# Kernel tuning notes

Hardware: AMD Instinct MI355X
Metric: run time of the kernel (lower is better)

The kernel has to match this reference:

```python
import jax, jax.numpy as jnp
import numpy as np

N = 100000   # nodes
E = 3200000  # edges (avg degree 32)
IN = 512
HID = 128
OUT = 128


def setup_inputs() -> dict:
    key = jax.random.key(0)
    ks = jax.random.split(key, 9)
    x = jax.random.normal(ks[0], (N, IN), dtype=jnp.float32)
    edge_index = jax.random.randint(ks[1], (2, E), 0, N, dtype=jnp.int32)
    perm = jax.random.permutation(ks[2], N).astype(jnp.int32)
    # GCN layer params (glorot-ish scaling)
    W1 = jax.random.normal(ks[3], (IN, HID), jnp.float32) / np.sqrt(IN)
    b1 = jnp.zeros((HID,), jnp.float32)
    W2 = jax.random.normal(ks[4], (HID, OUT), jnp.float32) / np.sqrt(HID)
    b2 = jnp.zeros((OUT,), jnp.float32)
    # nn.Bilinear(OUT, OUT, 1): weight [1, OUT, OUT], bias [1]
    Wd = jax.random.normal(ks[5], (1, OUT, OUT), jnp.float32) / np.sqrt(OUT)
    bd = jnp.zeros((1,), jnp.float32)
    return {"x": x, "edge_index": edge_index, "perm": perm,
            "W1": W1, "b1": b1, "W2": W2, "b2": b2, "Wd": Wd, "bd": bd}


def gcn_conv(x, W, b, src, dst, n):
    """PyG GCNConv: add self-loops, symmetric deg^-1/2 norm, linear, scatter-add, bias."""
    h = x @ W  # [N, out]
    loops = jnp.arange(n, dtype=src.dtype)
    s = jnp.concatenate([src, loops])
    d = jnp.concatenate([dst, loops])
    deg = jax.ops.segment_sum(jnp.ones(d.shape, x.dtype), d, num_segments=n)
    dinv = jnp.where(deg > 0, jax.lax.rsqrt(deg), 0.0)
    norm = dinv[s] * dinv[d]                      # [E+N]
    msg = h[s] * norm[:, None]                     # gather + scale
    out = jax.ops.segment_sum(msg, d, num_segments=n)  # scatter-add to dst
    return out + b


def encode(x, W1, b1, W2, b2, src, dst, n):
    h = jax.nn.relu(gcn_conv(x, W1, b1, src, dst, n))
    return gcn_conv(h, W2, b2, src, dst, n)


def reference(x, edge_index, perm, W1, b1, W2, b2, Wd, bd):
    n = x.shape[0]
    src, dst = edge_index[0], edge_index[1]
    H = encode(x, W1, b1, W2, b2, src, dst, n)          # [N, OUT]
    s = jax.nn.sigmoid(jnp.mean(H, axis=0))             # [OUT]
    # Bilinear disc against broadcasted summary: pos[n] = H[n] @ Wd[0] @ s + bd
    Ws = Wd[0] @ s                                      # [OUT]
    pos = (H @ Ws)[:, None] + bd                        # [N, 1]
    Hc = encode(x[perm], W1, b1, W2, b2, src, dst, n)
    neg = (Hc @ Ws)[:, None] + bd                       # [N, 1]
    return pos, neg
```

## Files before the change

kernel.cpp:

```cpp
#include <hip/hip_runtime.h>
#include <hip/hip_bf16.h>

typedef unsigned int uint;
typedef unsigned short ushort;
typedef __attribute__((ext_vector_type(8))) short bf16x8;
typedef __attribute__((ext_vector_type(4))) float f32x4;

static __device__ __forceinline__ ushort f2bf(float f) {
    uint u = __builtin_bit_cast(uint, f);
    return (ushort)((u + 0x7FFFu + ((u >> 16) & 1u)) >> 16);
}
static __device__ __forceinline__ uint pk2(float lo, float hi) {
    return (uint)f2bf(lo) | ((uint)f2bf(hi) << 16);
}
static __device__ __forceinline__ float bflo(uint u) { return __builtin_bit_cast(float, u << 16); }
static __device__ __forceinline__ float bfhi(uint u) { return __builtin_bit_cast(float, u & 0xFFFF0000u); }


#define CS_G 512

__global__ __launch_bounds__(256) void part_hist_dual(
        const int* __restrict__ src, const int* __restrict__ dst,
        uint* __restrict__ counts, int E, int NB, int chunk) {
    __shared__ uint h0[512], h1[512];
    int t = threadIdx.x;
    for (int b = t; b < 512; b += 256) { h0[b] = 0; h1[b] = 0; }
    __syncthreads();
    int s0 = blockIdx.x * chunk;
    int s1 = min(s0 + chunk, E);
    int i = s0 + t * 4;
    for (; i + 4 <= s1; i += 1024) {
        int4 d4 = *(const int4*)(dst + i);
        int4 s4 = *(const int4*)(src + i);
        atomicAdd(&h0[d4.x >> 8], 1u); atomicAdd(&h0[d4.y >> 8], 1u);
        atomicAdd(&h0[d4.z >> 8], 1u); atomicAdd(&h0[d4.w >> 8], 1u);
        atomicAdd(&h1[s4.x >> 8], 1u); atomicAdd(&h1[s4.y >> 8], 1u);
        atomicAdd(&h1[s4.z >> 8], 1u); atomicAdd(&h1[s4.w >> 8], 1u);
    }
    for (int k = i; k < min(i + 4, s1); ++k) {
        atomicAdd(&h0[dst[k] >> 8], 1u);
        atomicAdd(&h1[src[k] >> 8], 1u);
    }
    __syncthreads();
    for (int b = t; b < NB; b += 256) {
        counts[(size_t)b * CS_G + blockIdx.x] = h0[b];
        counts[(size_t)(NB + b) * CS_G + blockIdx.x] = h1[b];
    }
}

__global__ __launch_bounds__(256) void part_scatter_dual(
        const int* __restrict__ src, const int* __restrict__ dst,
        const uint* __restrict__ scn, uint* __restrict__ rec,
        int E, int NB, int chunk) {
    __shared__ uint cur0[512], cur1[512];
    int t = threadIdx.x;
    for (int b = t; b < NB; b += 256) {
        cur0[b] = scn[(size_t)b * CS_G + blockIdx.x];
        cur1[b] = scn[(size_t)(NB + b) * CS_G + blockIdx.x];
    }
    __syncthreads();
    int s0 = blockIdx.x * chunk;
    int s1 = min(s0 + chunk, E);
    int i = s0 + t * 4;
    for (; i + 4 <= s1; i += 1024) {
        int4 d4 = *(const int4*)(dst + i);
        int4 s4 = *(const int4*)(src + i);
        int dd[4] = {d4.x, d4.y, d4.z, d4.w};
        int ss[4] = {s4.x, s4.y, s4.z, s4.w};
#pragma unroll
        for (int k = 0; k < 4; ++k) {
            uint slotD = atomicAdd(&cur0[dd[k] >> 8], 1u);
            rec[slotD] = ((uint)(dd[k] & 255) << 24) | (uint)ss[k];
            uint slotS = atomicAdd(&cur1[ss[k] >> 8], 1u);
            rec[slotS] = ((uint)(ss[k] & 255) << 24) | (uint)dd[k];
        }
    }
    for (int k = i; k < min(i + 4, s1); ++k) {
        int d = dst[k], s = src[k];
        uint slotD = atomicAdd(&cur0[d >> 8], 1u);
        rec[slotD] = ((uint)(d & 255) << 24) | (uint)s;
        uint slotS = atomicAdd(&cur1[s >> 8], 1u);
        rec[slotS] = ((uint)(s & 255) << 24) | (uint)d;
    }
}

__global__ __launch_bounds__(256) void bucket_build(
        const uint* __restrict__ scn, const uint* __restrict__ rec,
        int* __restrict__ rp, int* __restrict__ adj,
        float* __restrict__ dinv, int NB, int n) {
    __shared__ uint cnt[256];
    __shared__ uint sc[2][256];
    int b = blockIdx.x, t = threadIdx.x;
    uint base = scn[(size_t)b * CS_G];
    uint bend = scn[(size_t)(b + 1) * CS_G];
    cnt[t] = 0;
    __syncthreads();
    for (uint i = base + t; i < bend; i += 256)
        atomicAdd(&cnt[rec[i] >> 24], 1u);
    __syncthreads();
    uint vcnt = cnt[t];
    float dv = rsqrtf((float)(vcnt + 1));
    sc[0][t] = vcnt;
    __syncthreads();
    int pb = 0;
    for (int off = 1; off < 256; off <<= 1) {
        uint add = (t >= off) ? sc[pb][t - off] : 0u;
        sc[pb ^ 1][t] = sc[pb][t] + add;
        pb ^= 1;
        __syncthreads();
    }
    uint excl = sc[pb][t] - vcnt;
    uint off0 = base + excl;
    int vtx = b * 256 + t;
    if (vtx < n) {
        rp[vtx] = (int)off0;
        dinv[vtx] = dv;
    }
    if (b == 0 && t == 0) rp[n] = (int)scn[(size_t)NB * CS_G];
    cnt[t] = off0;
    __syncthreads();
    for (uint i = base + t; i < bend; i += 256) {
        uint r = rec[i];
        uint slot = atomicAdd(&cnt[r >> 24], 1u);
        adj[slot] = (int)(r & 0xFFFFFFu);
    }
}

__global__ __launch_bounds__(256) void bucket_tw(
        const uint* __restrict__ scn, const uint* __restrict__ rec,
        const float* __restrict__ dinv, float* __restrict__ tv,
        int NB, int n) {
    __shared__ float tw_sh[256];
    int b = blockIdx.x, t = threadIdx.x;
    uint base = scn[(size_t)(NB + b) * CS_G];
    uint bend = scn[(size_t)(NB + b + 1) * CS_G];
    tw_sh[t] = 0.f;
    __syncthreads();
    for (uint i = base + t; i < bend; i += 256) {
        uint r = rec[i];
        atomicAdd(&tw_sh[r >> 24], dinv[r & 0xFFFFFFu]);
    }
    __syncthreads();
    int vtx = b * 256 + t;
    if (vtx < n) {
        float dv = dinv[vtx];
        tv[vtx] = dv * (tw_sh[t] + dv);
    }
}


#define SC_T 256
#define SC_C 1024

__global__ void scan_part(const int* __restrict__ deg, int* __restrict__ bsum, int n) {
    __shared__ int sh[SC_T];
    int t = threadIdx.x;
    int base = blockIdx.x * SC_C;
    int s = 0;
    for (int i = 0; i < 4; i++) {
        int idx = base + t * 4 + i;
        if (idx < n) s += deg[idx];
    }
    sh[t] = s;
    __syncthreads();
    for (int off = 128; off > 0; off >>= 1) {
        if (t < off) sh[t] += sh[t + off];
        __syncthreads();
    }
    if (t == 0) bsum[blockIdx.x] = sh[0];
}

__global__ void scan_block(int* bsum, int nb, int* total) {
    __shared__ int sh[256];
    int t = threadIdx.x;
    int v[4];
    int s = 0;
#pragma unroll
    for (int i = 0; i < 4; i++) {
        int idx = t * 4 + i;
        v[i] = (idx < nb) ? bsum[idx] : 0;
        s += v[i];
    }
    sh[t] = s;
    __syncthreads();
    for (int off = 1; off < 256; off <<= 1) {
        int u = (t >= off) ? sh[t - off] : 0;
        __syncthreads();
        sh[t] += u;
        __syncthreads();
    }
    int excl = sh[t] - s;
#pragma unroll
    for (int i = 0; i < 4; i++) {
        int idx = t * 4 + i;
        if (idx < nb) { bsum[idx] = excl; excl += v[i]; }
    }
    if (t == 255) *total = sh[255];
}

__global__ void scan_write(const int* __restrict__ deg, const int* __restrict__ bsum,
                           const int* __restrict__ total, int* __restrict__ rp, int n) {
    __shared__ int sh[SC_T];
    int t = threadIdx.x;
    int base = blockIdx.x * SC_C;
    int vals[4];
    int s = 0;
    for (int i = 0; i < 4; i++) {
        int idx = base + t * 4 + i;
        vals[i] = (idx < n) ? deg[idx] : 0;
        s += vals[i];
    }
    sh[t] = s;
    __syncthreads();
    for (int off = 1; off < SC_T; off <<= 1) {
        int v = (t >= off) ? sh[t - off] : 0;
        __syncthreads();
        sh[t] += v;
        __syncthreads();
    }
    int excl = sh[t] - s + bsum[blockIdx.x];
    for (int i = 0; i < 4; i++) {
        int idx = base + t * 4 + i;
        if (idx < n) { rp[idx] = excl; excl += vals[i]; }
    }
    if (blockIdx.x == 0 && t == 0) rp[n] = *total;
}


__global__ void pack_w(const float* __restrict__ W, ushort* __restrict__ Wp) {
    int kc = blockIdx.x >> 3, n = blockIdx.x & 7;
    int l = threadIdx.x;
    ushort o[8];
#pragma unroll
    for (int j = 0; j < 8; ++j) {
        float v = W[(size_t)(kc * 32 + ((l >> 4) * 8) + j) * 128 + n * 16 + (l & 15)];
        o[j] = f2bf(v);
    }
    uint4 pk;
    pk.x = (uint)o[0] | ((uint)o[1] << 16);
    pk.y = (uint)o[2] | ((uint)o[3] << 16);
    pk.z = (uint)o[4] | ((uint)o[5] << 16);
    pk.w = (uint)o[6] | ((uint)o[7] << 16);
    *(uint4*)(Wp + ((size_t)(kc * 8 + n) * 64 + l) * 8) = pk;
}


__global__ __launch_bounds__(256) void gemm1_mfma(
        const float* __restrict__ X, const ushort* __restrict__ Wp,
        ushort* __restrict__ Cb, int M, int K) {
    __shared__ ushort As[2][64][40];
    int t = threadIdx.x, lane = t & 63, w = t >> 6;
    int brow = blockIdx.x * 64;
    int KC = K >> 5;
    f32x4 acc[8] = {};
    int sr = t >> 2, sk = (t & 3) * 8;
    int gr = brow + sr;
    bool xok = gr < M;
    int frow = w * 16 + (lane & 15);
    int fk = (lane >> 4) * 8;

    auto loadpk = [&](int kc) -> uint4 {
        float4 xa = make_float4(0.f, 0.f, 0.f, 0.f), xb = xa;
        if (xok) {
            const float* xp = X + (size_t)gr * K + kc * 32 + sk;
            xa = *(const float4*)xp;
            xb = *(const float4*)(xp + 4);
        }
        uint4 pk;
        pk.x = pk2(xa.x, xa.y);
        pk.y = pk2(xa.z, xa.w);
        pk.z = pk2(xb.x, xb.y);
        pk.w = pk2(xb.z, xb.w);
        return pk;
    };

    uint4 cur = loadpk(0);
    int buf = 0;
    for (int kc = 0; kc < KC; ++kc) {
        *(uint4*)&As[buf][sr][sk] = cur;
        __syncthreads();
        if (kc + 1 < KC) cur = loadpk(kc + 1);
        bf16x8 af = *(const bf16x8*)&As[buf][frow][fk];
        const ushort* wbase = Wp + ((size_t)(kc * 8) * 64 + lane) * 8;
#pragma unroll
        for (int n = 0; n < 8; ++n) {
            bf16x8 bfr = *(const bf16x8*)(wbase + (size_t)n * 64 * 8);
            acc[n] = __builtin_amdgcn_mfma_f32_16x16x32_bf16(af, bfr, acc[n], 0, 0, 0);
        }
        buf ^= 1;
    }
    int colbase = lane & 15;
    int rowbase = brow + w * 16 + ((lane >> 4) << 2);
#pragma unroll
    for (int n = 0; n < 8; ++n) {
#pragma unroll
        for (int r = 0; r < 4; ++r) {
            int grr = rowbase + r;
            if (grr < M) Cb[(size_t)grr * 128 + n * 16 + colbase] = f2bf(acc[n][r]);
        }
    }
}


#define ACC8(acc, g, w)                                   \
    acc[0] += bflo(g.x) * w; acc[1] += bfhi(g.x) * w;     \
    acc[2] += bflo(g.y) * w; acc[3] += bfhi(g.y) * w;     \
    acc[4] += bflo(g.z) * w; acc[5] += bfhi(g.z) * w;     \
    acc[6] += bflo(g.w) * w; acc[7] += bfhi(g.w) * w;

__global__ __launch_bounds__(256) void prop_b0(
        const ushort* __restrict__ A,
        const int* __restrict__ rp, const int* __restrict__ adj,
        const float* __restrict__ dinv, const float* __restrict__ tv,
        const float* __restrict__ bias,
        ushort* __restrict__ B, float* __restrict__ mparts, int n) {
    __shared__ float msum[128];
    int t = threadIdx.x;
    if (t < 128) msum[t] = 0.f;
    __syncthreads();
    int wave = (blockIdx.x * blockDim.x + t) >> 6;
    int lane = t & 63;
    int q = lane >> 4, l = lane & 15;
    int v = wave * 4 + q;
    bool vok = v < n;
    int vc = vok ? v : (n - 1);
    float dv = dinv[vc];

    uint4 r0 = *(const uint4*)(A + (size_t)vc * 128 + 8 * l);
    float a0[8];
    a0[0] = bflo(r0.x) * dv; a0[1] = bfhi(r0.x) * dv;
    a0[2] = bflo(r0.y) * dv; a0[3] = bfhi(r0.y) * dv;
    a0[4] = bflo(r0.z) * dv; a0[5] = bfhi(r0.z) * dv;
    a0[6] = bflo(r0.w) * dv; a0[7] = bfhi(r0.w) * dv;

    int i = rp[vc], end = rp[vc + 1];
    int un[4];
#pragma unroll
    for (int k = 0; k < 4; ++k) un[k] = (i + k < end) ? adj[i + k] : vc;

    while (__ballot(i < end)) {
        int uc[4];
#pragma unroll
        for (int k = 0; k < 4; ++k) uc[k] = un[k];
        uint4 g0[4];
#pragma unroll
        for (int k = 0; k < 4; ++k) g0[k] = *(const uint4*)(A + (size_t)uc[k] * 128 + 8 * l);
        float du[4];
#pragma unroll
        for (int k = 0; k < 4; ++k) du[k] = (i + k < end) ? dinv[uc[k]] : 0.f;
        i += 4;
#pragma unroll
        for (int k = 0; k < 4; ++k) un[k] = (i + k < end) ? adj[i + k] : vc;
#pragma unroll
        for (int k = 0; k < 4; ++k) {
            float w = du[k];
            ACC8(a0, g0[k], w)
        }
    }
    float4 bA = *(const float4*)(bias + 8 * l);
    float4 bB = *(const float4*)(bias + 8 * l + 4);
    float bb[8] = {bA.x, bA.y, bA.z, bA.w, bB.x, bB.y, bB.z, bB.w};
#pragma unroll
    for (int j = 0; j < 8; ++j)
        a0[j] = fmaxf(a0[j] * dv + bb[j], 0.f);
    if (vok) {
        uint4 o;
        o.x = pk2(a0[0], a0[1]); o.y = pk2(a0[2], a0[3]);
        o.z = pk2(a0[4], a0[5]); o.w = pk2(a0[6], a0[7]);
        *(uint4*)(B + (size_t)v * 128 + 8 * l) = o;
    }
    float tvv = vok ? tv[vc] : 0.f;
#pragma unroll
    for (int j = 0; j < 8; ++j)
        atomicAdd(&msum[8 * l + j], tvv * a0[j]);
    __syncthreads();
    if (t < 128)
        atomicAdd(&mparts[(size_t)(blockIdx.x & 31) * 128 + t], msum[t]);
}


__global__ __launch_bounds__(256) void prop_b1(
        const ushort* __restrict__ A, const ushort* __restrict__ B,
        const int* __restrict__ rp, const int* __restrict__ adj,
        const float* __restrict__ dinv, const int* __restrict__ perm,
        const float* __restrict__ bias, const float* __restrict__ w2s,
        float2* __restrict__ cpair, int n) {
    int wave = (blockIdx.x * blockDim.x + threadIdx.x) >> 6;
    int lane = threadIdx.x & 63;
    int q = lane >> 4, l = lane & 15;
    int v = wave * 4 + q;
    bool vok = v < n;
    int vc = vok ? v : (n - 1);
    float dv = dinv[vc];
    int self = perm[vc];

    uint4 r1 = *(const uint4*)(A + (size_t)self * 128 + 8 * l);
    float a1[8];
    a1[0] = bflo(r1.x) * dv; a1[1] = bfhi(r1.x) * dv;
    a1[2] = bflo(r1.y) * dv; a1[3] = bfhi(r1.y) * dv;
    a1[4] = bflo(r1.z) * dv; a1[5] = bfhi(r1.z) * dv;
    a1[6] = bflo(r1.w) * dv; a1[7] = bfhi(r1.w) * dv;

    int i = rp[vc], end = rp[vc + 1];
    int un[4];
#pragma unroll
    for (int k = 0; k < 4; ++k) un[k] = (i + k < end) ? adj[i + k] : vc;

    while (__ballot(i < end)) {
        int uc[4];
#pragma unroll
        for (int k = 0; k < 4; ++k) uc[k] = un[k];
        int uu[4];
#pragma unroll
        for (int k = 0; k < 4; ++k) uu[k] = perm[uc[k]];
        uint4 g1[4];
#pragma unroll
        for (int k = 0; k < 4; ++k) g1[k] = *(const uint4*)(A + (size_t)uu[k] * 128 + 8 * l);
        float du[4];
#pragma unroll
        for (int k = 0; k < 4; ++k) du[k] = (i + k < end) ? dinv[uc[k]] : 0.f;
        i += 4;
#pragma unroll
        for (int k = 0; k < 4; ++k) un[k] = (i + k < end) ? adj[i + k] : vc;
#pragma unroll
        for (int k = 0; k < 4; ++k) {
            float w = du[k];
            ACC8(a1, g1[k], w)
        }
    }
    if (!vok) return;
    float4 bA = *(const float4*)(bias + 8 * l);
    float4 bB = *(const float4*)(bias + 8 * l + 4);
    float bb[8] = {bA.x, bA.y, bA.z, bA.w, bB.x, bB.y, bB.z, bB.w};
    float4 wA = *(const float4*)(w2s + 8 * l);
    float4 wB = *(const float4*)(w2s + 8 * l + 4);
    float ww[8] = {wA.x, wA.y, wA.z, wA.w, wB.x, wB.y, wB.z, wB.w};
    float c1 = 0.f;
#pragma unroll
    for (int j = 0; j < 8; ++j)
        c1 += fmaxf(a1[j] * dv + bb[j], 0.f) * ww[j];
    uint4 b0 = *(const uint4*)(B + (size_t)vc * 128 + 8 * l);
    float c0 = bflo(b0.x) * ww[0] + bfhi(b0.x) * ww[1]
             + bflo(b0.y) * ww[2] + bfhi(b0.y) * ww[3]
             + bflo(b0.z) * ww[4] + bfhi(b0.z) * ww[5]
             + bflo(b0.w) * ww[6] + bfhi(b0.w) * ww[7];
#pragma unroll
    for (int off = 1; off < 16; off <<= 1) {
        c0 += __shfl_xor(c0, off);
        c1 += __shfl_xor(c1, off);
    }
    if (l == 0) cpair[v] = make_float2(dv * c0, dv * c1);
}


__global__ void tiny_chain(const float* __restrict__ mparts, const float* __restrict__ W2,
                           const float* __restrict__ b2, const float* __restrict__ Wd,
                           const float* __restrict__ bd,
                           float* __restrict__ w2s, float* __restrict__ k0, int n) {
    __shared__ float mB[128];
    __shared__ float s_sh[128];
    __shared__ float ws_sh[128];
    __shared__ float red[128];
    int t = threadIdx.x;
    float acc = 0.f;
    for (int r = 0; r < 32; ++r) acc += mparts[(size_t)r * 128 + t];
    mB[t] = acc;
    __syncthreads();
    acc = 0.f;
    for (int k = 0; k < 128; ++k) acc += mB[k] * W2[k * 128 + t];
    float m = acc / (float)n + b2[t];
    s_sh[t] = 1.f / (1.f + expf(-m));
    __syncthreads();
    acc = 0.f;
    for (int j = 0; j < 128; ++j) acc += Wd[t * 128 + j] * s_sh[j];
    ws_sh[t] = acc;
    __syncthreads();
    acc = 0.f;
    for (int j = 0; j < 128; ++j) acc += W2[t * 128 + j] * ws_sh[j];
    w2s[t] = acc;
    red[t] = b2[t] * ws_sh[t];
    __syncthreads();
    for (int off = 64; off > 0; off >>= 1) {
        if (t < off) red[t] += red[t + off];
        __syncthreads();
    }
    if (t == 0) *k0 = red[0] + bd[0];
}

__global__ __launch_bounds__(256) void sprop(
        const float2* __restrict__ cpair,
        const int* __restrict__ rp, const int* __restrict__ adj,
        const float* __restrict__ dinv, const float* __restrict__ k0,
        float* __restrict__ out, int n) {
    int wave = (blockIdx.x * blockDim.x + threadIdx.x) >> 6;
    int lane = threadIdx.x & 63;
    int q = lane >> 4, l = lane & 15;
    int v = wave * 4 + q;
    if (v >= n) return;
    float a0 = 0.f, a1 = 0.f;
    int beg = rp[v], end = rp[v + 1];
    for (int i = beg + l; i < end; i += 16) {
        float2 c = cpair[adj[i]];
        a0 += c.x;
        a1 += c.y;
    }
#pragma unroll
    for (int off = 1; off < 16; off <<= 1) {
        a0 += __shfl_xor(a0, off);
        a1 += __shfl_xor(a1, off);
    }
    if (l == 0) {
        float dv = dinv[v];
        float kk = *k0;
        float2 cs = cpair[v];
        out[v] = dv * (a0 + cs.x) + kk;
        out[n + v] = dv * (a1 + cs.y) + kk;
    }
}


extern "C" void kernel_launch(void* const* d_in, const int* in_sizes, int n_in,
                              void* d_out, int out_size, void* d_ws, size_t ws_size,
                              hipStream_t stream) {
    const float* x  = (const float*)d_in[0];
    const int*   ei = (const int*)d_in[1];
    const int* perm = (const int*)d_in[2];
    const float* W1 = (const float*)d_in[3];
    const float* b1 = (const float*)d_in[4];
    const float* W2 = (const float*)d_in[5];
    const float* b2 = (const float*)d_in[6];
    const float* Wd = (const float*)d_in[7];
    const float* bd = (const float*)d_in[8];

    const int N = in_sizes[2];
    const int E = in_sizes[1] / 2;
    const int IN = in_sizes[0] / N;
    const int* src = ei;
    const int* dst = ei + E;
    float* out = (float*)d_out;

    const int NB = (N + 255) >> 8;
    const int M2 = 2 * NB * CS_G;
    int chunk = (E + CS_G - 1) / CS_G;
    chunk = (chunk + 3) & ~3;

    char* p = (char*)d_ws;
    auto alloc = [&](size_t bytes) -> void* {
        void* r = (void*)p;
        p += (bytes + 511) & ~(size_t)511;
        return r;
    };
    float* mparts = (float*)alloc(32 * 128 * 4);
    uint*  counts = (uint*)alloc((size_t)M2 * 4);
    uint*  scn    = (uint*)alloc((size_t)(M2 + 1) * 4);
    uint*  rec    = (uint*)alloc((size_t)2 * E * 4);
    int*   rp     = (int*)alloc((size_t)(N + 1) * 4);
    int*   adj    = (int*)alloc((size_t)E * 4);
    float* dinv   = (float*)alloc((size_t)N * 4);
    float* tvv    = (float*)alloc((size_t)N * 4);
    int*   bsum   = (int*)alloc(4096);
    int*   total  = (int*)alloc(64);
    float* w2sv   = (float*)alloc(512);
    float* k0v    = (float*)alloc(64);
    float2* cpair = (float2*)alloc((size_t)N * 8);
    ushort* W1p   = (ushort*)alloc((size_t)512 * 128 * 2);
    ushort* A  = (ushort*)alloc((size_t)N * 128 * 2);
    ushort* B  = (ushort*)alloc((size_t)N * 128 * 2);

    hipMemsetAsync(mparts, 0, 32 * 128 * 4, stream);

    part_hist_dual<<<CS_G, 256, 0, stream>>>(src, dst, counts, E, NB, chunk);
    int nb_sc = (M2 + SC_C - 1) / SC_C;
    scan_part<<<nb_sc, SC_T, 0, stream>>>((const int*)counts, bsum, M2);
    scan_block<<<1, 256, 0, stream>>>(bsum, nb_sc, total);
    scan_write<<<nb_sc, SC_T, 0, stream>>>((const int*)counts, bsum, total, (int*)scn, M2);
    part_scatter_dual<<<CS_G, 256, 0, stream>>>(src, dst, scn, rec, E, NB, chunk);
    bucket_build<<<NB, 256, 0, stream>>>(scn, rec, rp, adj, dinv, NB, N);
    bucket_tw<<<NB, 256, 0, stream>>>(scn, rec, dinv, tvv, NB, N);

    pack_w<<<(IN / 32) * 8, 64, 0, stream>>>(W1, W1p);

    int gemm_blocks = (N + 63) / 64;
    int p4_blocks = ((N + 3) / 4 + 3) / 4;

    gemm1_mfma<<<gemm_blocks, 256, 0, stream>>>(x, W1p, A, N, IN);
    prop_b0<<<p4_blocks, 256, 0, stream>>>(A, rp, adj, dinv, tvv, b1, B, mparts, N);
    tiny_chain<<<1, 128, 0, stream>>>(mparts, W2, b2, Wd, bd, w2sv, k0v, N);
    prop_b1<<<p4_blocks, 256, 0, stream>>>(A, B, rp, adj, dinv, perm, b1, w2sv, cpair, N);
    sprop<<<p4_blocks, 256, 0, stream>>>(cpair, rp, adj, dinv, k0v, out, N);
}
```

Measured before the change: 494.4 us.

## Process nodes in degree-sorted order and drop LDS staging in GEMM

Adds a counting sort of nodes by in-degree (histogram, scan, scatter) and makes the two propagation kernels process nodes in that order. Nodes sharing a wave then have similar neighbor counts, which is meant to cut divergence from uneven gather loop lengths. Separately, the first GEMM now loads X straight into MFMA fragments instead of staging through shared memory with barriers. The costs are three extra small kernels, scattered writes to B and cpair, and X loads whose pattern may coalesce less well without LDS.

```diff
diff --git a/kernel.cpp b/kernel.cpp
--- a/kernel.cpp
+++ b/kernel.cpp
@@ -87,7 +87,7 @@
 __global__ __launch_bounds__(256) void bucket_build(
         const uint* __restrict__ scn, const uint* __restrict__ rec,
         int* __restrict__ rp, int* __restrict__ adj,
-        float* __restrict__ dinv, int NB, int n) {
+        float* __restrict__ dinv, int* __restrict__ deg, int NB, int n) {
     __shared__ uint cnt[256];
     __shared__ uint sc[2][256];
     int b = blockIdx.x, t = threadIdx.x;
@@ -115,6 +115,7 @@
     if (vtx < n) {
         rp[vtx] = (int)off0;
         dinv[vtx] = dv;
+        deg[vtx] = (int)vcnt;
     }
     if (b == 0 && t == 0) rp[n] = (int)scn[(size_t)NB * CS_G];
     cnt[t] = off0;
@@ -149,6 +150,44 @@
 }
 
 
+__global__ __launch_bounds__(256) void deg_hist(
+        const int* __restrict__ deg, uint* __restrict__ gh, int n) {
+    __shared__ uint h[256];
+    int t = threadIdx.x;
+    h[t] = 0;
+    __syncthreads();
+    for (int i = blockIdx.x * 256 + t; i < n; i += gridDim.x * 256)
+        atomicAdd(&h[min(deg[i], 255)], 1u);
+    __syncthreads();
+    if (h[t]) atomicAdd(&gh[t], h[t]);
+}
+
+__global__ void deg_scan(const uint* __restrict__ gh, uint* __restrict__ gcur) {
+    __shared__ uint sh[256];
+    int t = threadIdx.x;
+    uint v = gh[t];
+    sh[t] = v;
+    __syncthreads();
+    for (int off = 1; off < 256; off <<= 1) {
+        uint u = (t >= off) ? sh[t - off] : 0u;
+        __syncthreads();
+        sh[t] += u;
+        __syncthreads();
+    }
+    gcur[t] = sh[t] - v;
+}
+
+__global__ __launch_bounds__(256) void deg_scatter(
+        const int* __restrict__ deg, uint* __restrict__ gcur,
+        int* __restrict__ nodeord, int n) {
+    int i = blockIdx.x * 256 + threadIdx.x;
+    if (i < n) {
+        uint pos = atomicAdd(&gcur[min(deg[i], 255)], 1u);
+        nodeord[pos] = i;
+    }
+}
+
+
 #define SC_T 256
 #define SC_C 1024
 
@@ -248,46 +287,31 @@
 __global__ __launch_bounds__(256) void gemm1_mfma(
         const float* __restrict__ X, const ushort* __restrict__ Wp,
         ushort* __restrict__ Cb, int M, int K) {
-    __shared__ ushort As[2][64][40];
     int t = threadIdx.x, lane = t & 63, w = t >> 6;
     int brow = blockIdx.x * 64;
     int KC = K >> 5;
+    int frow = brow + w * 16 + (lane & 15);
+    bool rok = frow < M;
+    const float* xrow = X + (size_t)(rok ? frow : 0) * K + ((lane >> 4) * 8);
     f32x4 acc[8] = {};
-    int sr = t >> 2, sk = (t & 3) * 8;
-    int gr = brow + sr;
-    bool xok = gr < M;
-    int frow = w * 16 + (lane & 15);
-    int fk = (lane >> 4) * 8;
-
-    auto loadpk = [&](int kc) -> uint4 {
+    for (int kc = 0; kc < KC; ++kc) {
         float4 xa = make_float4(0.f, 0.f, 0.f, 0.f), xb = xa;
-        if (xok) {
-            const float* xp = X + (size_t)gr * K + kc * 32 + sk;
-            xa = *(const float4*)xp;
-            xb = *(const float4*)(xp + 4);
+        if (rok) {
+            xa = *(const float4*)(xrow + kc * 32);
+            xb = *(const float4*)(xrow + kc * 32 + 4);
         }
         uint4 pk;
         pk.x = pk2(xa.x, xa.y);
         pk.y = pk2(xa.z, xa.w);
         pk.z = pk2(xb.x, xb.y);
         pk.w = pk2(xb.z, xb.w);
-        return pk;
-    };
-
-    uint4 cur = loadpk(0);
-    int buf = 0;
-    for (int kc = 0; kc < KC; ++kc) {
-        *(uint4*)&As[buf][sr][sk] = cur;
-        __syncthreads();
-        if (kc + 1 < KC) cur = loadpk(kc + 1);
-        bf16x8 af = *(const bf16x8*)&As[buf][frow][fk];
+        bf16x8 af = __builtin_bit_cast(bf16x8, pk);
         const ushort* wbase = Wp + ((size_t)(kc * 8) * 64 + lane) * 8;
 #pragma unroll
         for (int n = 0; n < 8; ++n) {
             bf16x8 bfr = *(const bf16x8*)(wbase + (size_t)n * 64 * 8);
             acc[n] = __builtin_amdgcn_mfma_f32_16x16x32_bf16(af, bfr, acc[n], 0, 0, 0);
         }
-        buf ^= 1;
     }
     int colbase = lane & 15;
     int rowbase = brow + w * 16 + ((lane >> 4) << 2);
@@ -309,7 +333,7 @@
     acc[6] += bflo(g.w) * w; acc[7] += bfhi(g.w) * w;
 
 __global__ __launch_bounds__(256) void prop_b0(
-        const ushort* __restrict__ A,
+        const ushort* __restrict__ A, const int* __restrict__ nodeord,
         const int* __restrict__ rp, const int* __restrict__ adj,
         const float* __restrict__ dinv, const float* __restrict__ tv,
         const float* __restrict__ bias,
@@ -321,9 +345,9 @@
     int wave = (blockIdx.x * blockDim.x + t) >> 6;
     int lane = t & 63;
     int q = lane >> 4, l = lane & 15;
-    int v = wave * 4 + q;
-    bool vok = v < n;
-    int vc = vok ? v : (n - 1);
+    int idx = wave * 4 + q;
+    bool vok = idx < n;
+    int vc = nodeord[vok ? idx : n - 1];
     float dv = dinv[vc];
 
     uint4 r0 = *(const uint4*)(A + (size_t)vc * 128 + 8 * l);
@@ -367,7 +391,7 @@
         uint4 o;
         o.x = pk2(a0[0], a0[1]); o.y = pk2(a0[2], a0[3]);
         o.z = pk2(a0[4], a0[5]); o.w = pk2(a0[6], a0[7]);
-        *(uint4*)(B + (size_t)v * 128 + 8 * l) = o;
+        *(uint4*)(B + (size_t)vc * 128 + 8 * l) = o;
     }
     float tvv = vok ? tv[vc] : 0.f;
 #pragma unroll
@@ -381,6 +405,7 @@
 
 __global__ __launch_bounds__(256) void prop_b1(
         const ushort* __restrict__ A, const ushort* __restrict__ B,
+        const int* __restrict__ nodeord,
         const int* __restrict__ rp, const int* __restrict__ adj,
         const float* __restrict__ dinv, const int* __restrict__ perm,
         const float* __restrict__ bias, const float* __restrict__ w2s,
@@ -388,9 +413,9 @@
     int wave = (blockIdx.x * blockDim.x + threadIdx.x) >> 6;
     int lane = threadIdx.x & 63;
     int q = lane >> 4, l = lane & 15;
-    int v = wave * 4 + q;
-    bool vok = v < n;
-    int vc = vok ? v : (n - 1);
+    int idx = wave * 4 + q;
+    bool vok = idx < n;
+    int vc = nodeord[vok ? idx : n - 1];
     float dv = dinv[vc];
     int self = perm[vc];
 
@@ -449,7 +474,7 @@
         c0 += __shfl_xor(c0, off);
         c1 += __shfl_xor(c1, off);
     }
-    if (l == 0) cpair[v] = make_float2(dv * c0, dv * c1);
+    if (l == 0) cpair[vc] = make_float2(dv * c0, dv * c1);
 }
 
 
@@ -551,6 +576,9 @@
         return r;
     };
     float* mparts = (float*)alloc(32 * 128 * 4);
+    uint*  gh     = (uint*)alloc(1024);
+    size_t zspan  = (size_t)((char*)p - (char*)mparts);
+    uint*  gcur   = (uint*)alloc(1024);
     uint*  counts = (uint*)alloc((size_t)M2 * 4);
     uint*  scn    = (uint*)alloc((size_t)(M2 + 1) * 4);
     uint*  rec    = (uint*)alloc((size_t)2 * E * 4);
@@ -558,6 +586,8 @@
     int*   adj    = (int*)alloc((size_t)E * 4);
     float* dinv   = (float*)alloc((size_t)N * 4);
     float* tvv    = (float*)alloc((size_t)N * 4);
+    int*   deg    = (int*)alloc((size_t)N * 4);
+    int*   nodeord= (int*)alloc((size_t)N * 4);
     int*   bsum   = (int*)alloc(4096);
     int*   total  = (int*)alloc(64);
     float* w2sv   = (float*)alloc(512);
@@ -567,7 +597,7 @@
     ushort* A  = (ushort*)alloc((size_t)N * 128 * 2);
     ushort* B  = (ushort*)alloc((size_t)N * 128 * 2);
 
-    hipMemsetAsync(mparts, 0, 32 * 128 * 4, stream);
+    hipMemsetAsync(mparts, 0, zspan, stream);
 
     part_hist_dual<<<CS_G, 256, 0, stream>>>(src, dst, counts, E, NB, chunk);
     int nb_sc = (M2 + SC_C - 1) / SC_C;
@@ -575,8 +605,12 @@
     scan_block<<<1, 256, 0, stream>>>(bsum, nb_sc, total);
     scan_write<<<nb_sc, SC_T, 0, stream>>>((const int*)counts, bsum, total, (int*)scn, M2);
     part_scatter_dual<<<CS_G, 256, 0, stream>>>(src, dst, scn, rec, E, NB, chunk);
-    bucket_build<<<NB, 256, 0, stream>>>(scn, rec, rp, adj, dinv, NB, N);
+    bucket_build<<<NB, 256, 0, stream>>>(scn, rec, rp, adj, dinv, deg, NB, N);
     bucket_tw<<<NB, 256, 0, stream>>>(scn, rec, dinv, tvv, NB, N);
+
+    deg_hist<<<128, 256, 0, stream>>>(deg, gh, N);
+    deg_scan<<<1, 256, 0, stream>>>(gh, gcur);
+    deg_scatter<<<(N + 255) / 256, 256, 0, stream>>>(deg, gcur, nodeord, N);
 
     pack_w<<<(IN / 32) * 8, 64, 0, stream>>>(W1, W1p);
 
@@ -584,8 +618,8 @@
     int p4_blocks = ((N + 3) / 4 + 3) / 4;
 
     gemm1_mfma<<<gemm_blocks, 256, 0, stream>>>(x, W1p, A, N, IN);
-    prop_b0<<<p4_blocks, 256, 0, stream>>>(A, rp, adj, dinv, tvv, b1, B, mparts, N);
+    prop_b0<<<p4_blocks, 256, 0, stream>>>(A, nodeord, rp, adj, dinv, tvv, b1, B, mparts, N);
     tiny_chain<<<1, 128, 0, stream>>>(mparts, W2, b2, Wd, bd, w2sv, k0v, N);
-    prop_b1<<<p4_blocks, 256, 0, stream>>>(A, B, rp, adj, dinv, perm, b1, w2sv, cpair, N);
+    prop_b1<<<p4_blocks, 256, 0, stream>>>(A, B, nodeord, rp, adj, dinv, perm, b1, w2sv, cpair, N);
     sprop<<<p4_blocks, 256, 0, stream>>>(cpair, rp, adj, dinv, k0v, out, N);
 }
```

Measured after the change: 683.1 us. +38.2%, slower.
